# Performance work log

Measured on AMD Instinct MI355X. Metric: run time of the kernel, lower is better.

The kernel has to match this reference:

```python
import jax, jax.numpy as jnp
import numpy as np

K = 9          # kernel points along H (morph=0 -> kernel shape (9,1))
PAD = K // 2   # same padding along H
EPS = 1e-5     # batchnorm eps


def setup_inputs() -> dict:
    key = jax.random.key(0)
    ks = jax.random.split(key, 6)
    B, Cin, Cout, H, W = 4, 64, 64, 160, 160
    x = jax.random.normal(ks[0], (B, Cin, H, W), jnp.float32)
    # offset branch conv: 2*K offset channels, kernel (K,1)
    w_off = jax.random.normal(ks[1], (2 * K, Cin, K, 1), jnp.float32) * 0.05
    b_off = jax.random.normal(ks[2], (2 * K,), jnp.float32) * 0.05
    gamma = jnp.ones((2 * K,), jnp.float32)
    beta = jnp.zeros((2 * K,), jnp.float32)
    # deformable conv weights: kernel (K,1), groups=1
    w_def = jax.random.normal(ks[3], (Cout, Cin, K, 1), jnp.float32) * 0.05
    b_def = jax.random.normal(ks[4], (Cout,), jnp.float32) * 0.05
    return {"x": x, "w_off": w_off, "b_off": b_off, "gamma": gamma,
            "beta": beta, "w_def": w_def, "b_def": b_def}


def _convert_offsets(off):
    # morph=0: even channels (x) -> 0; odd channels (y) -> per-kernel-point cumsum
    c = K // 2
    y = off[:, 1::2]                                            # [B,K,H,W]
    top = jnp.flip(jnp.cumsum(jnp.flip(y[:, :c + 1], 1), 1), 1)  # suffix-cumsum to center
    bot = jnp.cumsum(jnp.concatenate([top[:, c:c + 1], y[:, c + 1:]], 1), 1)
    y_new = jnp.concatenate([top[:, :c], bot], 1)
    return jnp.zeros_like(off).at[:, 1::2].set(y_new)


def _deform_conv(x, off, w, b):
    B, C, H, W = x.shape
    dy = off[:, 0::2]                                           # [B,K,H,W]
    dx = off[:, 1::2]
    ky = jnp.arange(K, dtype=x.dtype).reshape(1, K, 1, 1)
    py = jnp.arange(H, dtype=x.dtype).reshape(1, 1, H, 1) - PAD + ky + dy
    px = jnp.arange(W, dtype=x.dtype).reshape(1, 1, 1, W) + dx
    y0 = jnp.floor(py)
    x0 = jnp.floor(px)
    fy = py - y0
    fx = px - x0
    y0i = y0.astype(jnp.int32)
    x0i = x0.astype(jnp.int32)
    xf = x.reshape(B, C, H * W)

    def gather(yc, xc):
        # zero-padded bilinear corner gather -> [B,C,K,H,W]
        valid = ((yc >= 0) & (yc < H) & (xc >= 0) & (xc < W)).astype(x.dtype)
        lin = jnp.clip(yc, 0, H - 1) * W + jnp.clip(xc, 0, W - 1)
        v = jax.vmap(lambda img, idx: img[:, idx])(xf, lin)
        return v * valid[:, None]

    w00 = ((1 - fy) * (1 - fx))[:, None]
    w01 = ((1 - fy) * fx)[:, None]
    w10 = (fy * (1 - fx))[:, None]
    w11 = (fy * fx)[:, None]
    samples = (w00 * gather(y0i, x0i) + w01 * gather(y0i, x0i + 1)
               + w10 * gather(y0i + 1, x0i) + w11 * gather(y0i + 1, x0i + 1))
    # contract kernel points and input channels
    return jnp.einsum('bckhw,ock->bohw', samples, w[:, :, :, 0]) + b[None, :, None, None]


def reference(x, w_off, b_off, gamma, beta, w_def, b_def):
    # offset branch: conv -> batchnorm (training-mode stats) -> tanh -> snake cumsum
    off = jax.lax.conv_general_dilated(
        x, w_off, (1, 1), ((PAD, PAD), (0, 0)),
        dimension_numbers=('NCHW', 'OIHW', 'NCHW')) + b_off[None, :, None, None]
    mu = off.mean((0, 2, 3), keepdims=True)
    var = off.var((0, 2, 3), keepdims=True)
    off = (off - mu) * jax.lax.rsqrt(var + EPS) * gamma[None, :, None, None] + beta[None, :, None, None]
    off = _convert_offsets(jnp.tanh(off))
    return _deform_conv(x, off, w_def, b_def)
```

## Files before the change

kernel.cpp:

```cpp
#include <hip/hip_runtime.h>
#include <hip/hip_fp16.h>
#include <math.h>

#define HW    25600
#define WID   160
#define HEI   160
#define BB    4
#define CIN   64
#define COUT  64
#define NBN   102400
#define TSTR  162

typedef _Float16 f16x8 __attribute__((ext_vector_type(8)));
typedef float    f32x4 __attribute__((ext_vector_type(4)));

union U4 { int i[4]; f16x8 v; };
union HU { unsigned u; __half2 h; };

__device__ __forceinline__ unsigned short f2h(float f) {
    return __half_as_ushort(__float2half(f));
}

__device__ __forceinline__ float ftanh(float x) {
    float e = __builtin_amdgcn_exp2f(x * 2.8853900817779268f);
    return 1.0f - 2.0f * __builtin_amdgcn_rcpf(e + 1.0f);
}

__global__ __launch_bounds__(256) void p0_prep(
        const float* __restrict__ x, const float* __restrict__ w_def,
        const float* __restrict__ w_off,
        unsigned short* __restrict__ xbT, unsigned short* __restrict__ wtA,
        unsigned short* __restrict__ wofA, float* __restrict__ stats) {
    int t = threadIdx.x;
    int blk = blockIdx.x;
    if (blk == 640) {
        for (int u = 0; u < 144; ++u) {
            int idx = t + u * 256;
            int k = idx >> 12;
            int r = idx & 4095;
            int chalf = r >> 11;
            int og = (r >> 9) & 3;
            int L = (r >> 3) & 63;
            int j = idx & 7;
            int o = og * 16 + (L & 15);
            int c = chalf * 32 + (L >> 4) * 8 + j;
            wtA[idx] = f2h(w_def[(o * CIN + c) * 9 + k]);
        }
        for (int u = 0; u < 36; ++u) {
            int idx = t + u * 256;
            int jj = idx & 7;
            int L  = (idx >> 3) & 63;
            int ch = (idx >> 9) & 1;
            int k  = idx >> 10;
            int j  = L & 15;
            int c  = ch * 32 + (L >> 4) * 8 + jj;
            wofA[idx] = (j < 9) ? f2h(w_off[((2 * j + 1) * CIN + c) * 9 + k])
                                : (unsigned short)0;
        }
        if (t < 32) stats[t] = 0.f;
        return;
    }
    __shared__ __align__(16) unsigned short tile[CIN * TSTR];
    int b = blk / HEI, h = blk % HEI;
    const float* xp = x + (b * CIN) * HW + h * WID;
    unsigned* ti = (unsigned*)tile;
#pragma unroll
    for (int u = 0; u < 10; ++u) {
        int e = t + u * 256;
        int c = e / 40, wq = e - c * 40;
        const float4 v = *(const float4*)(xp + c * HW + 4 * wq);
        unsigned p01 = f2h(v.x) | ((unsigned)f2h(v.y) << 16);
        unsigned p23 = f2h(v.z) | ((unsigned)f2h(v.w) << 16);
        ti[81 * c + 2 * wq]     = p01;
        ti[81 * c + 2 * wq + 1] = p23;
    }
    __syncthreads();
    unsigned* dst = (unsigned*)(xbT + (b * HEI + h) * (WID * 64));
#pragma unroll
    for (int u = 0; u < 20; ++u) {
        int e = t + u * 256;
        int w = e >> 5, cp = e & 31;
        unsigned lo = tile[(2 * cp) * TSTR + w];
        unsigned hi = tile[(2 * cp + 1) * TSTR + w];
        dst[e] = lo | (hi << 16);
    }
}

__global__ __launch_bounds__(320) void k1_offconv_mfma(
        const unsigned short* __restrict__ xbT,
        const unsigned short* __restrict__ wofA,
        const float* __restrict__ b_off,
        float* __restrict__ off_odd, float* __restrict__ stats) {
    int t = threadIdx.x;
    int blk = blockIdx.x;
    int xcd = blk & 7;
    int idx = blk >> 3;
    int b   = idx / 40;
    int r2  = idx - b * 40;
    int h   = xcd * 20 + (r2 >> 1);
    int p0  = (r2 & 1) * 80;
    int wave = t >> 6, lane = t & 63;
    int l15 = lane & 15, q = lane >> 4;
    int px  = p0 + wave * 16 + l15;

    f32x4 acc = (f32x4){0.f, 0.f, 0.f, 0.f};

    int klo = 4 - h;   if (klo < 0) klo = 0;
    int khi = 163 - h; if (khi > 8) khi = 8;

    for (int k = klo; k <= khi; ++k) {
        int py = h + k - 4;
        const unsigned short* sp = xbT + (b * HEI + py) * (WID * 64) + px * 64;
        f16x8 a0 = *(const f16x8*)(wofA + ((k * 2 + 0) * 64 + lane) * 8);
        f16x8 a1 = *(const f16x8*)(wofA + ((k * 2 + 1) * 64 + lane) * 8);
        f16x8 b0 = *(const f16x8*)(sp + q * 8);
        f16x8 b1 = *(const f16x8*)(sp + 32 + q * 8);
        acc = __builtin_amdgcn_mfma_f32_16x16x32_f16(a0, b0, acc, 0, 0, 0);
        acc = __builtin_amdgcn_mfma_f32_16x16x32_f16(a1, b1, acc, 0, 0, 0);
    }

    float sS[4] = {0.f, 0.f, 0.f, 0.f}, sQ[4] = {0.f, 0.f, 0.f, 0.f};
#pragma unroll
    for (int r = 0; r < 4; ++r) {
        int j = q * 4 + r;
        if (j < 9) {
            float v = acc[r] + b_off[2 * j + 1];
            off_odd[(b * 9 + j) * HW + h * WID + px] = v;
            sS[r] = v; sQ[r] = v * v;
        }
    }
#pragma unroll
    for (int o = 1; o < 16; o <<= 1) {
#pragma unroll
        for (int r = 0; r < 4; ++r) {
            sS[r] += __shfl_xor(sS[r], o);
            sQ[r] += __shfl_xor(sQ[r], o);
        }
    }
    __shared__ float redS[5][16], redQ[5][16];
    if (l15 == 0) {
#pragma unroll
        for (int r = 0; r < 4; ++r) {
            int j = q * 4 + r;
            if (j < 9) { redS[wave][j] = sS[r]; redQ[wave][j] = sQ[r]; }
        }
    }
    __syncthreads();
    if (t < 18) {
        int j = (t < 9) ? t : t - 9;
        float v = 0.f;
#pragma unroll
        for (int w = 0; w < 5; ++w)
            v += (t < 9) ? redS[w][j] : redQ[w][j];
        atomicAdd(&stats[t], v);
    }
}

__global__ __launch_bounds__(256, 5) void k4_deform_mfma(
        const unsigned short* __restrict__ xbT,
        const float* __restrict__ off_odd,
        const float* __restrict__ stats,
        const float* __restrict__ gamma,
        const float* __restrict__ beta,
        const unsigned short* __restrict__ wtA,
        const float* __restrict__ b_def,
        float* __restrict__ out) {
    __shared__ __align__(16) int S[2][80 * 36];
    __shared__ unsigned P0h[9][80], P1h[9][80];
    __shared__ int      PXI[9][80];

    int t   = threadIdx.x;
    int blk = blockIdx.x;
    int xcd = blk & 7;
    int idx = blk >> 3;
    int b   = idx / 40;
    int r2  = idx - b * 40;
    int h   = xcd * 20 + (r2 >> 1);
    int p0  = (r2 & 1) * 80;
    int wave = t >> 6, lane = t & 63;
    int l15 = lane & 15, q = lane >> 4;

    if (t < 80) {
        int px = p0 + t;
        float tv[9];
#pragma unroll
        for (int j = 0; j < 9; ++j) {
            float mean = stats[j] * (1.0f / NBN);
            float var  = stats[9 + j] * (1.0f / NBN) - mean * mean;
            float inv  = rsqrtf(var + 1e-5f);
            float v = off_odd[(b * 9 + j) * HW + h * WID + px];
            tv[j] = ftanh((v - mean) * inv * gamma[2 * j + 1] + beta[2 * j + 1]);
        }
        float dxv[9];
        dxv[4] = tv[4];
#pragma unroll
        for (int i = 5; i < 9; ++i) dxv[i] = dxv[i - 1] + tv[i];
#pragma unroll
        for (int i = 3; i >= 0; --i) dxv[i] = dxv[i + 1] + tv[i];
#pragma unroll
        for (int j = 0; j < 9; ++j) {
            int py = h + j - 4;
            bool rowok = (py >= 0) && (py < HEI);
            float pxf = (float)px + dxv[j];
            float x0f = floorf(pxf);
            float fx  = pxf - x0f;
            int   x0  = (int)x0f;
            float s0f = (rowok && x0 >= 0 && x0 < WID) ? 1.f - fx : 0.f;
            float s1f = (rowok && x0 >= -1 && x0 < WID - 1) ? fx : 0.f;
            unsigned h0 = f2h(s0f), h1 = f2h(s1f);
            P0h[j][t] = h0 | (h0 << 16);
            P1h[j][t] = h1 | (h1 << 16);
            int xi0 = min(max(x0, 0), WID - 1);
            int xi1 = min(max(x0 + 1, 0), WID - 1);
            PXI[j][t] = xi0 | (xi1 << 16);
        }
    }
    __syncthreads();

    f32x4 acc[5];
#pragma unroll
    for (int i = 0; i < 5; ++i) acc[i] = (f32x4){0.f, 0.f, 0.f, 0.f};

    int4     A4[3], B4[3];
    unsigned sa[3], sb[3];
    f16x8    wpa, wpb;

#define PF(kk)                                                                  \
    {                                                                           \
        int pyc = min(max(h + (kk) - 4, 0), HEI - 1);                           \
        const int4* rowI4 = (const int4*)(xbT + (b * HEI + pyc) * (WID * 64));  \
        _Pragma("unroll")                                                       \
        for (int u = 0; u < 3; ++u) {                                           \
            if (u < 2 || t < 128) {                                             \
                int id = t + u * 256;                                           \
                int pxl = id >> 3, c4 = id & 7;                                 \
                int xi = PXI[kk][pxl];                                          \
                sa[u] = P0h[kk][pxl];                                           \
                sb[u] = P1h[kk][pxl];                                           \
                A4[u] = rowI4[(xi & 0xffff) * 8 + c4];                          \
                B4[u] = rowI4[(xi >> 16) * 8 + c4];                             \
            }                                                                   \
        }                                                                       \
        wpa = *(const f16x8*)(wtA + ((((kk) * 2 + 0) * 4 + wave) * 64 + lane) * 8); \
        wpb = *(const f16x8*)(wtA + ((((kk) * 2 + 1) * 4 + wave) * 64 + lane) * 8); \
    }

    PF(0);
    int buf = 0;

    for (int k = 0; k < 9; ++k) {
        int* Sb = S[buf];
#pragma unroll
        for (int u = 0; u < 3; ++u) {
            if (u < 2 || t < 128) {
                int id = t + u * 256;
                int pxl = id >> 3, c4 = id & 7;
                HU sah, sbh; sah.u = sa[u]; sbh.u = sb[u];
                int4 r4;
                HU a, bb, r;
#pragma unroll
                for (int ii = 0; ii < 4; ++ii) {
                    a.u  = (unsigned)(&A4[u].x)[ii];
                    bb.u = (unsigned)(&B4[u].x)[ii];
                    r.h  = __hfma2(sbh.h, bb.h, __hmul2(sah.h, a.h));
                    (&r4.x)[ii] = (int)r.u;
                }
                *(int4*)(Sb + pxl * 36 + (c4 << 2)) = r4;
            }
        }
        __syncthreads();

        f16x8 wf0 = wpa, wf1 = wpb;
        if (k < 8) PF(k + 1);

#pragma unroll
        for (int pxt = 0; pxt < 5; ++pxt) {
            const int* sp = &Sb[(pxt * 16 + l15) * 36];
            U4 u0, u1;
            *(int4*)u0.i = *(const int4*)(sp + q * 4);
            *(int4*)u1.i = *(const int4*)(sp + 16 + q * 4);
            acc[pxt] = __builtin_amdgcn_mfma_f32_16x16x32_f16(wf0, u0.v, acc[pxt], 0, 0, 0);
            acc[pxt] = __builtin_amdgcn_mfma_f32_16x16x32_f16(wf1, u1.v, acc[pxt], 0, 0, 0);
        }
        buf ^= 1;
    }
#undef PF

    float bd[4];
#pragma unroll
    for (int r = 0; r < 4; ++r) bd[r] = b_def[wave * 16 + q * 4 + r];
#pragma unroll
    for (int pxt = 0; pxt < 5; ++pxt) {
#pragma unroll
        for (int r = 0; r < 4; ++r) {
            int o = wave * 16 + q * 4 + r;
            out[(b * COUT + o) * HW + h * WID + p0 + pxt * 16 + l15] = acc[pxt][r] + bd[r];
        }
    }
}

extern "C" void kernel_launch(void* const* d_in, const int* in_sizes, int n_in,
                              void* d_out, int out_size, void* d_ws, size_t ws_size,
                              hipStream_t stream) {
    const float* x     = (const float*)d_in[0];
    const float* w_off = (const float*)d_in[1];
    const float* b_off = (const float*)d_in[2];
    const float* gamma = (const float*)d_in[3];
    const float* beta  = (const float*)d_in[4];
    const float* w_def = (const float*)d_in[5];
    const float* b_def = (const float*)d_in[6];
    float* out = (float*)d_out;

    float* off_odd       = (float*)d_ws;
    float* stats         = off_odd + 921600;
    unsigned short* wtA  = (unsigned short*)(stats + 32);
    unsigned short* wofA = wtA + 36864;
    unsigned short* xbT  = wofA + 9216;

    p0_prep<<<641, 256, 0, stream>>>(x, w_def, w_off, xbT, wtA, wofA, stats);
    k1_offconv_mfma<<<1280, 320, 0, stream>>>(xbT, wofA, b_off, off_odd, stats);
    k4_deform_mfma<<<1280, 256, 0, stream>>>(xbT, off_odd, stats, gamma, beta,
                                             wtA, b_def, out);
}
```

Baseline: 153.1 us.

## Compute deform samples directly in MFMA registers, dropping LDS staging

The deformable conv kernel now gives each of 5 waves 16 pixels. Each lane gathers and bilinearly blends its own channel fragments straight into the MFMA B operand and loops over all 64 output channels. This removes the double-buffered LDS sample tile and the per-kernel-point __syncthreads, and moves the launch to 320 threads. The cost is that weights are reloaded from global or cache per wave, there is no explicit prefetch of the next kernel point, and gathers are redundant across output-channel groups.

Result: slower. 174.8 us (+14.2%).

```diff
diff --git a/kernel.cpp b/kernel.cpp
--- a/kernel.cpp
+++ b/kernel.cpp
@@ -14,7 +14,7 @@
 typedef _Float16 f16x8 __attribute__((ext_vector_type(8)));
 typedef float    f32x4 __attribute__((ext_vector_type(4)));
 
-union U4 { int i[4]; f16x8 v; };
+union U4 { int i[4]; int4 v4; f16x8 v; };
 union HU { unsigned u; __half2 h; };
 
 __device__ __forceinline__ unsigned short f2h(float f) {
@@ -156,7 +156,7 @@
     }
 }
 
-__global__ __launch_bounds__(256, 5) void k4_deform_mfma(
+__global__ __launch_bounds__(320, 4) void k4_deform_mfma(
         const unsigned short* __restrict__ xbT,
         const float* __restrict__ off_odd,
         const float* __restrict__ stats,
@@ -165,7 +165,6 @@
         const unsigned short* __restrict__ wtA,
         const float* __restrict__ b_def,
         float* __restrict__ out) {
-    __shared__ __align__(16) int S[2][80 * 36];
     __shared__ unsigned P0h[9][80], P1h[9][80];
     __shared__ int      PXI[9][80];
 
@@ -217,84 +216,56 @@
     }
     __syncthreads();
 
-    f32x4 acc[5];
-#pragma unroll
-    for (int i = 0; i < 5; ++i) acc[i] = (f32x4){0.f, 0.f, 0.f, 0.f};
-
-    int4     A4[3], B4[3];
-    unsigned sa[3], sb[3];
-    f16x8    wpa, wpb;
-
-#define PF(kk)                                                                  \
-    {                                                                           \
-        int pyc = min(max(h + (kk) - 4, 0), HEI - 1);                           \
-        const int4* rowI4 = (const int4*)(xbT + (b * HEI + pyc) * (WID * 64));  \
-        _Pragma("unroll")                                                       \
-        for (int u = 0; u < 3; ++u) {                                           \
-            if (u < 2 || t < 128) {                                             \
-                int id = t + u * 256;                                           \
-                int pxl = id >> 3, c4 = id & 7;                                 \
-                int xi = PXI[kk][pxl];                                          \
-                sa[u] = P0h[kk][pxl];                                           \
-                sb[u] = P1h[kk][pxl];                                           \
-                A4[u] = rowI4[(xi & 0xffff) * 8 + c4];                          \
-                B4[u] = rowI4[(xi >> 16) * 8 + c4];                             \
-            }                                                                   \
-        }                                                                       \
-        wpa = *(const f16x8*)(wtA + ((((kk) * 2 + 0) * 4 + wave) * 64 + lane) * 8); \
-        wpb = *(const f16x8*)(wtA + ((((kk) * 2 + 1) * 4 + wave) * 64 + lane) * 8); \
-    }
-
-    PF(0);
-    int buf = 0;
-
+    int pxl = wave * 16 + l15;
+    f32x4 acc[4];
+#pragma unroll
+    for (int i = 0; i < 4; ++i) acc[i] = (f32x4){0.f, 0.f, 0.f, 0.f};
+
+    const int4* xb4 = (const int4*)xbT + (size_t)(b * HEI) * (WID * 8);
+    const f16x8* wA = (const f16x8*)wtA;
+
+#pragma unroll
     for (int k = 0; k < 9; ++k) {
-        int* Sb = S[buf];
-#pragma unroll
-        for (int u = 0; u < 3; ++u) {
-            if (u < 2 || t < 128) {
-                int id = t + u * 256;
-                int pxl = id >> 3, c4 = id & 7;
-                HU sah, sbh; sah.u = sa[u]; sbh.u = sb[u];
-                int4 r4;
-                HU a, bb, r;
-#pragma unroll
-                for (int ii = 0; ii < 4; ++ii) {
-                    a.u  = (unsigned)(&A4[u].x)[ii];
-                    bb.u = (unsigned)(&B4[u].x)[ii];
-                    r.h  = __hfma2(sbh.h, bb.h, __hmul2(sah.h, a.h));
-                    (&r4.x)[ii] = (int)r.u;
-                }
-                *(int4*)(Sb + pxl * 36 + (c4 << 2)) = r4;
-            }
-        }
-        __syncthreads();
-
-        f16x8 wf0 = wpa, wf1 = wpb;
-        if (k < 8) PF(k + 1);
-
-#pragma unroll
-        for (int pxt = 0; pxt < 5; ++pxt) {
-            const int* sp = &Sb[(pxt * 16 + l15) * 36];
-            U4 u0, u1;
-            *(int4*)u0.i = *(const int4*)(sp + q * 4);
-            *(int4*)u1.i = *(const int4*)(sp + 16 + q * 4);
-            acc[pxt] = __builtin_amdgcn_mfma_f32_16x16x32_f16(wf0, u0.v, acc[pxt], 0, 0, 0);
-            acc[pxt] = __builtin_amdgcn_mfma_f32_16x16x32_f16(wf1, u1.v, acc[pxt], 0, 0, 0);
-        }
-        buf ^= 1;
-    }
-#undef PF
-
-    float bd[4];
-#pragma unroll
-    for (int r = 0; r < 4; ++r) bd[r] = b_def[wave * 16 + q * 4 + r];
-#pragma unroll
-    for (int pxt = 0; pxt < 5; ++pxt) {
+        int pyc = min(max(h + k - 4, 0), HEI - 1);
+        const int4* row = xb4 + pyc * (WID * 8);
+
+        int xi = PXI[k][pxl];
+        HU sa, sb; sa.u = P0h[k][pxl]; sb.u = P1h[k][pxl];
+        int i0 = (xi & 0xffff) * 8 + q;
+        int i1 = (xi >> 16) * 8 + q;
+
+        U4 A0, B0, A1, B1;
+        A0.v4 = row[i0];     B0.v4 = row[i1];
+        A1.v4 = row[i0 + 4]; B1.v4 = row[i1 + 4];
+
+        U4 f0, f1;
+#pragma unroll
+        for (int ii = 0; ii < 4; ++ii) {
+            HU a, bb, r;
+            a.u = (unsigned)A0.i[ii]; bb.u = (unsigned)B0.i[ii];
+            r.h = __hfma2(sb.h, bb.h, __hmul2(sa.h, a.h));
+            f0.i[ii] = (int)r.u;
+            a.u = (unsigned)A1.i[ii]; bb.u = (unsigned)B1.i[ii];
+            r.h = __hfma2(sb.h, bb.h, __hmul2(sa.h, a.h));
+            f1.i[ii] = (int)r.u;
+        }
+
+        const f16x8* wk0 = wA + (k * 2 + 0) * 256 + lane;
+        const f16x8* wk1 = wA + (k * 2 + 1) * 256 + lane;
+#pragma unroll
+        for (int og = 0; og < 4; ++og)
+            acc[og] = __builtin_amdgcn_mfma_f32_16x16x32_f16(wk0[og * 64], f0.v, acc[og], 0, 0, 0);
+#pragma unroll
+        for (int og = 0; og < 4; ++og)
+            acc[og] = __builtin_amdgcn_mfma_f32_16x16x32_f16(wk1[og * 64], f1.v, acc[og], 0, 0, 0);
+    }
+
+#pragma unroll
+    for (int og = 0; og < 4; ++og) {
 #pragma unroll
         for (int r = 0; r < 4; ++r) {
-            int o = wave * 16 + q * 4 + r;
-            out[(b * COUT + o) * HW + h * WID + p0 + pxt * 16 + l15] = acc[pxt][r] + bd[r];
+            int o = og * 16 + q * 4 + r;
+            out[(b * COUT + o) * HW + h * WID + p0 + pxl] = acc[og][r] + b_def[o];
         }
     }
 }
@@ -319,6 +290,6 @@
 
     p0_prep<<<641, 256, 0, stream>>>(x, w_def, w_off, xbT, wtA, wofA, stats);
     k1_offconv_mfma<<<1280, 320, 0, stream>>>(xbT, wofA, b_off, off_odd, stats);
-    k4_deform_mfma<<<1280, 256, 0, stream>>>(xbT, off_odd, stats, gamma, beta,
+    k4_deform_mfma<<<1280, 320, 0, stream>>>(xbT, off_odd, stats, gamma, beta,
                                              wtA, b_def, out);
 }
```
